# Optimization experiments

Measured on AMD Instinct MI355X. Metric: run time of the kernel, lower is better.

Reference implementation:

```python
import jax, jax.numpy as jnp
import numpy as np

NUM_LAYERS = 4
D_MODEL = 1024
N_HEAD = 16
D_FF = 1024
BATCH = 2
LONG = 2048
SHORT = 256


def setup_inputs() -> dict:
    key = jax.random.key(0)
    ks = jax.random.split(key, 6)
    s = 0.02
    L, D, F = NUM_LAYERS, D_MODEL, D_FF
    S = LONG + SHORT
    return {
        "x": jax.random.normal(ks[0], (BATCH, S, D), jnp.float32),
        "Wqkv": jax.random.normal(ks[1], (L, 3 * D, D), jnp.float32) * s,
        "bqkv": jnp.zeros((L, 3 * D), jnp.float32),
        "Wo": jax.random.normal(ks[2], (L, D, D), jnp.float32) * s,
        "bo": jnp.zeros((L, D), jnp.float32),
        "W1": jax.random.normal(ks[3], (L, F, D), jnp.float32) * s,
        "b1": jnp.zeros((L, F), jnp.float32),
        "W2": jax.random.normal(ks[4], (L, D, F), jnp.float32) * s,
        "b2": jnp.zeros((L, D), jnp.float32),
        "ln1_w": jnp.ones((L, D), jnp.float32),
        "ln1_b": jnp.zeros((L, D), jnp.float32),
        "ln2_w": jnp.ones((L, D), jnp.float32),
        "ln2_b": jnp.zeros((L, D), jnp.float32),
        "norm_w": jnp.ones((D,), jnp.float32),
        "norm_b": jnp.zeros((D,), jnp.float32),
        "long_seq_length": LONG,
        "num_short_seqs": SHORT,
    }


def _ln(x, w, b, eps=1e-5):
    m = jnp.mean(x, axis=-1, keepdims=True)
    v = jnp.mean(jnp.square(x - m), axis=-1, keepdims=True)
    return (x - m) * jax.lax.rsqrt(v + eps) * w + b


def _build_mask(long_seq_length, num_short_seqs, dtype):
    S = long_seq_length + num_short_seqs
    # long rows: attend only to long cols; short rows: long cols + own diag
    allowed = jnp.zeros((S, S), bool).at[:, :long_seq_length].set(True)
    sidx = jnp.arange(long_seq_length, S)
    allowed = allowed.at[sidx, sidx].set(True)
    return jnp.where(allowed, jnp.zeros((), dtype), -jnp.inf).astype(dtype)


def reference(x, Wqkv, bqkv, Wo, bo, W1, b1, W2, b2,
              ln1_w, ln1_b, ln2_w, ln2_b, norm_w, norm_b,
              long_seq_length, num_short_seqs):
    # dropout layers are treated as identity (eval / deterministic)
    B, S, D = x.shape
    H = N_HEAD
    dh = D // H
    scale = 1.0 / np.sqrt(dh)
    mask = _build_mask(long_seq_length, num_short_seqs, x.dtype)  # [S,S]

    for l in range(Wqkv.shape[0]):
        # --- nn.TransformerEncoderLayer (post-norm) ---
        qkv = jnp.einsum('bsd,ed->bse', x, Wqkv[l]) + bqkv[l]  # [B,S,3D]
        q, k, v = jnp.split(qkv, 3, axis=-1)
        q = q.reshape(B, S, H, dh).transpose(0, 2, 1, 3)
        k = k.reshape(B, S, H, dh).transpose(0, 2, 1, 3)
        v = v.reshape(B, S, H, dh).transpose(0, 2, 1, 3)
        scores = jnp.einsum('bhsd,bhtd->bhst', q, k) * scale + mask
        attn = jax.nn.softmax(scores, axis=-1)
        ctx = jnp.einsum('bhst,bhtd->bhsd', attn, v)
        ctx = ctx.transpose(0, 2, 1, 3).reshape(B, S, D)
        attn_out = jnp.einsum('bsd,ed->bse', ctx, Wo[l]) + bo[l]
        h = _ln(x + attn_out, ln1_w[l], ln1_b[l])
        ff = jnp.einsum('bsf,df->bsd',
                        jax.nn.relu(jnp.einsum('bsd,fd->bsf', h, W1[l]) + b1[l]),
                        W2[l]) + b2[l]
        y = _ln(h + ff, ln2_w[l], ln2_b[l])
        # --- outer residual + shared LayerNorm ---
        x = _ln(x + y, norm_w, norm_b)
    return x
```

## Files before the change

kernel.cpp:

```cpp
#include <hip/hip_runtime.h>

#define DEV __device__ __forceinline__

typedef short bf16x8 __attribute__((ext_vector_type(8)));
typedef short bf16x4_t __attribute__((ext_vector_type(4)));
typedef float f32x4 __attribute__((ext_vector_type(4)));

#define S_TOT 2304
#define D3    3072
#define NLONG 2048

DEV unsigned short f2b(float f) {
    union { float f; unsigned u; } v; v.f = f;
    unsigned r = v.u + 0x7fffu + ((v.u >> 16) & 1u);
    return (unsigned short)(r >> 16);
}
DEV float b2f(unsigned short u) {
    union { unsigned u; float f; } v; v.u = ((unsigned)u) << 16;
    return v.f;
}

#define GLL16(g, l) __builtin_amdgcn_global_load_lds( \
    (const __attribute__((address_space(1))) void*)(g), \
    (__attribute__((address_space(3))) void*)(l), 16, 0, 0)

DEV bf16x4_t tr_read(unsigned byteaddr) {
    bf16x4_t r;
    asm volatile("ds_read_b64_tr_b16 %0, %1" : "=v"(r) : "v"(byteaddr));
    return r;
}

__global__ __launch_bounds__(256) void k_cast(const float* __restrict__ in,
                                              unsigned short* __restrict__ out, long n) {
    long i = ((long)blockIdx.x * 256 + threadIdx.x) * 4;
    long stride = (long)gridDim.x * 1024;
    for (; i < n; i += stride) {
        float4 v = *(const float4*)(in + i);
        *(ushort4*)(out + i) = make_ushort4(f2b(v.x), f2b(v.y), f2b(v.z), f2b(v.w));
    }
}

__global__ __launch_bounds__(256) void k_castcopy(const float* __restrict__ in,
                                                  float* __restrict__ outf,
                                                  unsigned short* __restrict__ outb, long n) {
    long i = ((long)blockIdx.x * 256 + threadIdx.x) * 4;
    long stride = (long)gridDim.x * 1024;
    for (; i < n; i += stride) {
        float4 v = *(const float4*)(in + i);
        *(float4*)(outf + i) = v;
        *(ushort4*)(outb + i) = make_ushort4(f2b(v.x), f2b(v.y), f2b(v.z), f2b(v.w));
    }
}

template<int BN, int OBF, int RELU>
__global__ __launch_bounds__(256, 2) void k_gemm(const unsigned short* __restrict__ A,
                                                 const unsigned short* __restrict__ B,
                                                 const float* __restrict__ bias,
                                                 float* __restrict__ Cf,
                                                 unsigned short* __restrict__ Cb,
                                                 int M, int N, int K) {
    __shared__ unsigned short As[2][128 * 32];
    __shared__ unsigned short Bs[2][BN * 32];
    const int tid  = threadIdx.x;
    const int lane = tid & 63;
    const int wave = tid >> 6;
    const int g = lane >> 4, li = lane & 15;
    const int bm = blockIdx.x, bn = blockIdx.y;
    constexpr int WN = BN / 2;
    constexpr int NF = WN / 16;
    const int wm = (wave >> 1) * 64, wn = (wave & 1) * WN;

    f32x4 acc[4][NF] = {};

    const long abase = (long)bm * 128 * K;
    const long bbase = (long)bn * BN * K;
    const int srow = tid >> 2;
    const int scol = (tid & 3) * 8;

    auto stage = [&](int kt, int buf) {
        GLL16(A + abase + (long)srow * K + kt + scol, As[buf] + tid * 8);
        GLL16(A + abase + (long)(srow + 64) * K + kt + scol, As[buf] + (tid + 256) * 8);
        GLL16(B + bbase + (long)srow * K + kt + scol, Bs[buf] + tid * 8);
        if (BN == 128)
            GLL16(B + bbase + (long)(srow + 64) * K + kt + scol, Bs[buf] + (tid + 256) * 8);
    };

    const int nt = K / 32;
    stage(0, 0);
    for (int t = 0; t < nt; ++t) {
        __syncthreads();
        if (t + 1 < nt) stage((t + 1) * 32, (t + 1) & 1);
        const unsigned short* Ab = As[t & 1];
        const unsigned short* Bb = Bs[t & 1];
        bf16x8 af[4], bfr[NF];
#pragma unroll
        for (int mf = 0; mf < 4; ++mf)
            af[mf] = *(const bf16x8*)(Ab + (wm + mf * 16 + li) * 32 + g * 8);
#pragma unroll
        for (int nf = 0; nf < NF; ++nf)
            bfr[nf] = *(const bf16x8*)(Bb + (wn + nf * 16 + li) * 32 + g * 8);
#pragma unroll
        for (int mf = 0; mf < 4; ++mf)
#pragma unroll
            for (int nf = 0; nf < NF; ++nf)
                acc[mf][nf] = __builtin_amdgcn_mfma_f32_16x16x32_bf16(af[mf], bfr[nf], acc[mf][nf], 0, 0, 0);
    }

#pragma unroll
    for (int nf = 0; nf < NF; ++nf) {
        int col = bn * BN + wn + nf * 16 + li;
        float bv = bias[col];
#pragma unroll
        for (int mf = 0; mf < 4; ++mf) {
#pragma unroll
            for (int i = 0; i < 4; ++i) {
                int row = bm * 128 + wm + mf * 16 + g * 4 + i;
                float v = acc[mf][nf][i] + bv;
                if (RELU) v = fmaxf(v, 0.f);
                if (OBF) Cb[(long)row * N + col] = f2b(v);
                else     Cf[(long)row * N + col] = v;
            }
        }
    }
}

__global__ __launch_bounds__(256, 2) void k_attn(const unsigned short* __restrict__ qkv,
                                                 unsigned short* __restrict__ ctx) {
    __shared__ unsigned short Ks[2][64 * 64];
    __shared__ unsigned short Vt[2][64 * 72];
    __shared__ unsigned short Ps[4][2048];

    const int tid  = threadIdx.x;
    const int lane = tid & 63, wave = tid >> 6;
    const int g = lane >> 4, li = lane & 15;
    const int bq = blockIdx.x, h = blockIdx.y, b = blockIdx.z;
    const int q0 = bq * 128 + wave * 32;

    const long baseQ = ((long)b * S_TOT) * D3 + h * 64;
    const long baseK = baseQ + 1024;
    const long baseV = baseQ + 2048;

    bf16x8 qf[2][2];
#pragma unroll
    for (int mf = 0; mf < 2; ++mf)
#pragma unroll
        for (int kk = 0; kk < 2; ++kk)
            qf[mf][kk] = *(const bf16x8*)(qkv + baseQ + (long)(q0 + mf * 16 + li) * D3 + kk * 32 + g * 8);

    f32x4 O[2][4] = {};
    float psum[2][4] = {};

    unsigned short* Pw = Ps[wave];
    const unsigned pwb = (unsigned)(size_t)Pw + lane * 8u;

    auto stageK = [&](int kt, int buf) {
#pragma unroll
        for (int r = 0; r < 2; ++r) {
            int s = tid + r * 256;
            int kr = s >> 3, si = s & 7;
            GLL16(qkv + baseK + (long)(kt + kr) * D3 + ((si ^ (kr & 7)) * 8), Ks[buf] + s * 8);
        }
    };
    auto loadV = [&](int kt, ushort4* vr) {
        int t0 = (tid & 15) * 4, d0 = (tid >> 4) * 4;
        const unsigned short* vp = qkv + baseV + (long)(kt + t0) * D3 + d0;
        vr[0] = *(const ushort4*)(vp);
        vr[1] = *(const ushort4*)(vp + D3);
        vr[2] = *(const ushort4*)(vp + 2 * D3);
        vr[3] = *(const ushort4*)(vp + 3 * D3);
    };
    auto writeVt = [&](const ushort4* vr, int buf) {
        int t0 = (tid & 15) * 4, d0 = (tid >> 4) * 4;
        unsigned short* Vb = Vt[buf];
        *(ushort4*)(Vb + (d0 + 0) * 72 + t0) = make_ushort4(vr[0].x, vr[1].x, vr[2].x, vr[3].x);
        *(ushort4*)(Vb + (d0 + 1) * 72 + t0) = make_ushort4(vr[0].y, vr[1].y, vr[2].y, vr[3].y);
        *(ushort4*)(Vb + (d0 + 2) * 72 + t0) = make_ushort4(vr[0].z, vr[1].z, vr[2].z, vr[3].z);
        *(ushort4*)(Vb + (d0 + 3) * 72 + t0) = make_ushort4(vr[0].w, vr[1].w, vr[2].w, vr[3].w);
    };

    auto compute = [&](int cur) {
        f32x4 sc[2][4] = {};
        const unsigned short* Kb = Ks[cur];
#pragma unroll
        for (int kk = 0; kk < 2; ++kk) {
            bf16x8 kf[4];
#pragma unroll
            for (int nf = 0; nf < 4; ++nf) {
                int kr = nf * 16 + li;
                int slot = (kk * 4 + g) ^ (kr & 7);
                kf[nf] = *(const bf16x8*)(Kb + kr * 64 + slot * 8);
            }
#pragma unroll
            for (int mf = 0; mf < 2; ++mf)
#pragma unroll
                for (int nf = 0; nf < 4; ++nf)
                    sc[mf][nf] = __builtin_amdgcn_mfma_f32_16x16x32_bf16(qf[mf][kk], kf[nf], sc[mf][nf], 0, 0, 0);
        }
#pragma unroll
        for (int mf = 0; mf < 2; ++mf) {
#pragma unroll
            for (int nf = 0; nf < 4; ++nf) {
                float p0 = __expf(sc[mf][nf][0] * 0.125f);
                float p1 = __expf(sc[mf][nf][1] * 0.125f);
                float p2 = __expf(sc[mf][nf][2] * 0.125f);
                float p3 = __expf(sc[mf][nf][3] * 0.125f);
                psum[mf][0] += p0; psum[mf][1] += p1;
                psum[mf][2] += p2; psum[mf][3] += p3;
                unsigned lo, hi;
                asm("v_cvt_pk_bf16_f32 %0, %1, %2" : "=v"(lo) : "v"(p0), "v"(p1));
                asm("v_cvt_pk_bf16_f32 %0, %1, %2" : "=v"(hi) : "v"(p2), "v"(p3));
                unsigned idx = (unsigned)(g * 4 + (li & 3) * 16 + (nf * 2 + (li >> 3)) * 64 +
                                          ((li >> 2) & 1) * 512 + mf * 1024);
                *(uint2*)(Pw + idx) = make_uint2(lo, hi);
            }
        }
        asm volatile("" ::: "memory");
        bf16x4_t pa[2][2][2];
#pragma unroll
        for (int mf = 0; mf < 2; ++mf)
#pragma unroll
            for (int kk = 0; kk < 2; ++kk) {
                unsigned base = pwb + 2u * (unsigned)(kk * 256 + mf * 1024);
                pa[mf][kk][0] = tr_read(base);
                pa[mf][kk][1] = tr_read(base + 1024u);
            }
        asm volatile("s_waitcnt lgkmcnt(0)" ::: "memory");
        __builtin_amdgcn_sched_barrier(0);
        const unsigned short* Vb = Vt[cur];
#pragma unroll
        for (int kk = 0; kk < 2; ++kk) {
            bf16x8 vf[4];
#pragma unroll
            for (int nfd = 0; nfd < 4; ++nfd)
                vf[nfd] = *(const bf16x8*)(Vb + (nfd * 16 + li) * 72 + kk * 32 + g * 8);
#pragma unroll
            for (int mf = 0; mf < 2; ++mf) {
                bf16x8 paf = __builtin_shufflevector(pa[mf][kk][0], pa[mf][kk][1],
                                                     0, 1, 2, 3, 4, 5, 6, 7);
#pragma unroll
                for (int nfd = 0; nfd < 4; ++nfd)
                    O[mf][nfd] = __builtin_amdgcn_mfma_f32_16x16x32_bf16(paf, vf[nfd], O[mf][nfd], 0, 0, 0);
            }
        }
    };

    ushort4 vrA[4], vrB[4];
    stageK(0, 0);
    loadV(0, vrA);
    for (int ti = 0; ti < 32; ti += 2) {
        writeVt(vrA, 0);
        __syncthreads();
        if (ti + 1 < 32) { stageK((ti + 1) * 64, 1); loadV((ti + 1) * 64, vrB); }
        compute(0);
        writeVt(vrB, 1);
        __syncthreads();
        if (ti + 2 < 32) { stageK((ti + 2) * 64, 0); loadV((ti + 2) * 64, vrA); }
        compute(1);
    }

    float lrow[2][4];
#pragma unroll
    for (int mf = 0; mf < 2; ++mf)
#pragma unroll
        for (int i = 0; i < 4; ++i) {
            float s = psum[mf][i];
#pragma unroll
            for (int off = 1; off < 16; off <<= 1) s += __shfl_xor(s, off);
            lrow[mf][i] = s;
        }

    if (q0 >= NLONG) {
#pragma unroll
        for (int mf = 0; mf < 2; ++mf) {
#pragma unroll
            for (int i = 0; i < 4; ++i) {
                int q = q0 + mf * 16 + g * 4 + i;
                ushort4 q4 = *(const ushort4*)(qkv + baseQ + (long)q * D3 + li * 4);
                ushort4 k4 = *(const ushort4*)(qkv + baseK + (long)q * D3 + li * 4);
                float p = b2f(q4.x) * b2f(k4.x) + b2f(q4.y) * b2f(k4.y) +
                          b2f(q4.z) * b2f(k4.z) + b2f(q4.w) * b2f(k4.w);
#pragma unroll
                for (int off = 1; off < 16; off <<= 1) p += __shfl_xor(p, off);
                float pe = __expf(p * 0.125f);
                lrow[mf][i] += pe;
#pragma unroll
                for (int nfd = 0; nfd < 4; ++nfd) {
                    float vd = b2f(qkv[baseV + (long)q * D3 + nfd * 16 + li]);
                    O[mf][nfd][i] += pe * vd;
                }
            }
        }
    }

#pragma unroll
    for (int mf = 0; mf < 2; ++mf) {
#pragma unroll
        for (int i = 0; i < 4; ++i) {
            float inv = 1.0f / lrow[mf][i];
            int q = q0 + mf * 16 + g * 4 + i;
            long obase = ((long)b * S_TOT + q) * 1024 + h * 64;
#pragma unroll
            for (int nfd = 0; nfd < 4; ++nfd)
                ctx[obase + nfd * 16 + li] = f2b(O[mf][nfd][i] * inv);
        }
    }
}

DEV void block_reduce2(float& sum, float& sq, float* sbuf, int tid) {
#pragma unroll
    for (int off = 32; off > 0; off >>= 1) {
        sum += __shfl_xor(sum, off);
        sq  += __shfl_xor(sq, off);
    }
    __syncthreads();
    if ((tid & 63) == 0) { sbuf[(tid >> 6) * 2] = sum; sbuf[(tid >> 6) * 2 + 1] = sq; }
    __syncthreads();
    sum = sbuf[0] + sbuf[2] + sbuf[4] + sbuf[6];
    sq  = sbuf[1] + sbuf[3] + sbuf[5] + sbuf[7];
}

__global__ __launch_bounds__(256) void k_ln_resid(const float* __restrict__ xa,
                                                  const float* __restrict__ xb,
                                                  const float* __restrict__ w,
                                                  const float* __restrict__ bs,
                                                  float* __restrict__ outf,
                                                  unsigned short* __restrict__ outb) {
    __shared__ float sbuf[8];
    const int tid = threadIdx.x;
    const long base = (long)blockIdx.x * 1024 + tid * 4;
    float4 a = *(const float4*)(xa + base);
    float4 b4 = *(const float4*)(xb + base);
    float4 s = make_float4(a.x + b4.x, a.y + b4.y, a.z + b4.z, a.w + b4.w);
    float sum = s.x + s.y + s.z + s.w;
    float sq = s.x * s.x + s.y * s.y + s.z * s.z + s.w * s.w;
    block_reduce2(sum, sq, sbuf, tid);
    float mean = sum * (1.f / 1024.f);
    float rstd = rsqrtf(sq * (1.f / 1024.f) - mean * mean + 1e-5f);
    float4 wv = *(const float4*)(w + tid * 4);
    float4 bv = *(const float4*)(bs + tid * 4);
    float4 o = make_float4((s.x - mean) * rstd * wv.x + bv.x,
                           (s.y - mean) * rstd * wv.y + bv.y,
                           (s.z - mean) * rstd * wv.z + bv.z,
                           (s.w - mean) * rstd * wv.w + bv.w);
    *(float4*)(outf + base) = o;
    *(ushort4*)(outb + base) = make_ushort4(f2b(o.x), f2b(o.y), f2b(o.z), f2b(o.w));
}

__global__ __launch_bounds__(256) void k_ln_double(const float* __restrict__ h,
                                                   const float* __restrict__ ff,
                                                   const float* __restrict__ x,
                                                   const float* __restrict__ w2,
                                                   const float* __restrict__ bb2,
                                                   const float* __restrict__ nw,
                                                   const float* __restrict__ nb,
                                                   float* __restrict__ outf,
                                                   unsigned short* __restrict__ outb) {
    __shared__ float sbuf[8];
    const int tid = threadIdx.x;
    const long base = (long)blockIdx.x * 1024 + tid * 4;
    float4 hv = *(const float4*)(h + base);
    float4 fv = *(const float4*)(ff + base);
    float4 s = make_float4(hv.x + fv.x, hv.y + fv.y, hv.z + fv.z, hv.w + fv.w);
    float sum = s.x + s.y + s.z + s.w;
    float sq = s.x * s.x + s.y * s.y + s.z * s.z + s.w * s.w;
    block_reduce2(sum, sq, sbuf, tid);
    float mean = sum * (1.f / 1024.f);
    float rstd = rsqrtf(sq * (1.f / 1024.f) - mean * mean + 1e-5f);
    float4 wv = *(const float4*)(w2 + tid * 4);
    float4 bv = *(const float4*)(bb2 + tid * 4);
    float4 y = make_float4((s.x - mean) * rstd * wv.x + bv.x,
                           (s.y - mean) * rstd * wv.y + bv.y,
                           (s.z - mean) * rstd * wv.z + bv.z,
                           (s.w - mean) * rstd * wv.w + bv.w);
    float4 xv = *(const float4*)(x + base);
    float4 t = make_float4(xv.x + y.x, xv.y + y.y, xv.z + y.z, xv.w + y.w);
    sum = t.x + t.y + t.z + t.w;
    sq = t.x * t.x + t.y * t.y + t.z * t.z + t.w * t.w;
    block_reduce2(sum, sq, sbuf, tid);
    mean = sum * (1.f / 1024.f);
    rstd = rsqrtf(sq * (1.f / 1024.f) - mean * mean + 1e-5f);
    float4 nwv = *(const float4*)(nw + tid * 4);
    float4 nbv = *(const float4*)(nb + tid * 4);
    float4 o = make_float4((t.x - mean) * rstd * nwv.x + nbv.x,
                           (t.y - mean) * rstd * nwv.y + nbv.y,
                           (t.z - mean) * rstd * nwv.z + nbv.z,
                           (t.w - mean) * rstd * nwv.w + nbv.w);
    *(float4*)(outf + base) = o;
    *(ushort4*)(outb + base) = make_ushort4(f2b(o.x), f2b(o.y), f2b(o.z), f2b(o.w));
}

extern "C" void kernel_launch(void* const* d_in, const int* in_sizes, int n_in,
                              void* d_out, int out_size, void* d_ws, size_t ws_size,
                              hipStream_t stream) {
    (void)in_sizes; (void)n_in; (void)out_size; (void)ws_size;
    const float* x_in  = (const float*)d_in[0];
    const float* Wqkv  = (const float*)d_in[1];
    const float* bqkv  = (const float*)d_in[2];
    const float* Wo    = (const float*)d_in[3];
    const float* bo    = (const float*)d_in[4];
    const float* W1    = (const float*)d_in[5];
    const float* b1    = (const float*)d_in[6];
    const float* W2    = (const float*)d_in[7];
    const float* b2    = (const float*)d_in[8];
    const float* ln1w  = (const float*)d_in[9];
    const float* ln1b  = (const float*)d_in[10];
    const float* ln2w  = (const float*)d_in[11];
    const float* ln2b  = (const float*)d_in[12];
    const float* nw    = (const float*)d_in[13];
    const float* nb    = (const float*)d_in[14];
    float* xf = (float*)d_out;

    char* p = (char*)d_ws;
    auto alloc = [&](size_t bytes) { char* r = p; p += (bytes + 255) & ~(size_t)255; return r; };
    unsigned short* wqkv_b = (unsigned short*)alloc(12582912UL * 2);
    unsigned short* wo_b   = (unsigned short*)alloc(4194304UL * 2);
    unsigned short* w1_b   = (unsigned short*)alloc(4194304UL * 2);
    unsigned short* w2_b   = (unsigned short*)alloc(4194304UL * 2);
    unsigned short* x_b    = (unsigned short*)alloc(4718592UL * 2);
    unsigned short* qkv_b  = (unsigned short*)alloc(14155776UL * 2);
    unsigned short* ctx_b  = (unsigned short*)alloc(4718592UL * 2);
    unsigned short* h_b    = (unsigned short*)alloc(4718592UL * 2);
    unsigned short* ff1_b  = (unsigned short*)alloc(4718592UL * 2);
    float* h_f   = (float*)alloc(4718592UL * 4);
    float* tmp_f = (float*)alloc(4718592UL * 4);

    k_cast<<<4096, 256, 0, stream>>>(Wqkv, wqkv_b, 12582912L);
    k_cast<<<2048, 256, 0, stream>>>(Wo, wo_b, 4194304L);
    k_cast<<<2048, 256, 0, stream>>>(W1, w1_b, 4194304L);
    k_cast<<<2048, 256, 0, stream>>>(W2, w2_b, 4194304L);
    k_castcopy<<<2048, 256, 0, stream>>>(x_in, xf, x_b, 4718592L);

    for (int l = 0; l < 4; ++l) {
        k_gemm<128, 1, 0><<<dim3(36, 24), 256, 0, stream>>>(x_b, wqkv_b + (size_t)l * 3145728,
                                                            bqkv + l * 3072, nullptr, qkv_b, 4608, 3072, 1024);
        k_attn<<<dim3(18, 16, 2), 256, 0, stream>>>(qkv_b, ctx_b);
        k_gemm<64, 0, 0><<<dim3(36, 16), 256, 0, stream>>>(ctx_b, wo_b + (size_t)l * 1048576,
                                                           bo + l * 1024, tmp_f, nullptr, 4608, 1024, 1024);
        k_ln_resid<<<4608, 256, 0, stream>>>(xf, tmp_f, ln1w + l * 1024, ln1b + l * 1024, h_f, h_b);
        k_gemm<64, 1, 1><<<dim3(36, 16), 256, 0, stream>>>(h_b, w1_b + (size_t)l * 1048576,
                                                           b1 + l * 1024, nullptr, ff1_b, 4608, 1024, 1024);
        k_gemm<64, 0, 0><<<dim3(36, 16), 256, 0, stream>>>(ff1_b, w2_b + (size_t)l * 1048576,
                                                           b2 + l * 1024, tmp_f, nullptr, 4608, 1024, 1024);
        k_ln_double<<<4608, 256, 0, stream>>>(h_f, tmp_f, xf, ln2w + l * 1024, ln2b + l * 1024,
                                              nw, nb, xf, x_b);
    }
}
```

Before: 1.149 ms.

## Split-K attention with combine kernel, triple-buffer GEMM, and swizzle workgroup order

The attention kernel now splits the 2048 long keys into two chunks across more blocks. It writes unnormalised partial outputs and row sums, and a new combine kernel merges them and adds the short-sequence diagonal term. V is now loaded straight into LDS with global_load_lds and read with transposed LDS reads, which replaces the register transpose. The GEMM moves to a 3-stage LDS pipeline with explicit vmcnt waits, higher occupancy hints and an XCD-aware block ID remap. Together these aim to raise parallelism and overlap memory with MFMA work, at the cost of extra fp32 partial traffic, which reuses the h_f/tmp_f buffers.

```diff
diff --git a/kernel.cpp b/kernel.cpp
--- a/kernel.cpp
+++ b/kernel.cpp
@@ -9,6 +9,7 @@
 #define S_TOT 2304
 #define D3    3072
 #define NLONG 2048
+#define OSTRIDE 4718592L
 
 DEV unsigned short f2b(float f) {
     union { float f; unsigned u; } v; v.f = f;
@@ -53,19 +54,26 @@
 }
 
 template<int BN, int OBF, int RELU>
-__global__ __launch_bounds__(256, 2) void k_gemm(const unsigned short* __restrict__ A,
-                                                 const unsigned short* __restrict__ B,
-                                                 const float* __restrict__ bias,
-                                                 float* __restrict__ Cf,
-                                                 unsigned short* __restrict__ Cb,
-                                                 int M, int N, int K) {
-    __shared__ unsigned short As[2][128 * 32];
-    __shared__ unsigned short Bs[2][BN * 32];
+__global__ __launch_bounds__(256, BN == 128 ? 3 : 4)
+void k_gemm(const unsigned short* __restrict__ A,
+            const unsigned short* __restrict__ B,
+            const float* __restrict__ bias,
+            float* __restrict__ Cf,
+            unsigned short* __restrict__ Cb,
+            int M, int N, int K) {
+    __shared__ unsigned short As[3][128 * 32];
+    __shared__ unsigned short Bs[3][BN * 32];
     const int tid  = threadIdx.x;
     const int lane = tid & 63;
     const int wave = tid >> 6;
     const int g = lane >> 4, li = lane & 15;
-    const int bm = blockIdx.x, bn = blockIdx.y;
+
+    const int nbm = gridDim.x;
+    const int nwg = nbm * gridDim.y;
+    int id = blockIdx.x + blockIdx.y * nbm;
+    if ((nwg & 7) == 0) id = (id & 7) * (nwg >> 3) + (id >> 3);
+    const int bm = id % nbm, bn = id / nbm;
+
     constexpr int WN = BN / 2;
     constexpr int NF = WN / 16;
     const int wm = (wave >> 1) * 64, wn = (wave & 1) * WN;
@@ -87,11 +95,17 @@
 
     const int nt = K / 32;
     stage(0, 0);
+    stage(32, 1);
+    if constexpr (BN == 128) asm volatile("s_waitcnt vmcnt(4)" ::: "memory");
+    else                     asm volatile("s_waitcnt vmcnt(3)" ::: "memory");
+
     for (int t = 0; t < nt; ++t) {
-        __syncthreads();
-        if (t + 1 < nt) stage((t + 1) * 32, (t + 1) & 1);
-        const unsigned short* Ab = As[t & 1];
-        const unsigned short* Bb = Bs[t & 1];
+        __builtin_amdgcn_s_barrier();
+        __builtin_amdgcn_sched_barrier(0);
+        asm volatile("" ::: "memory");
+        if (t + 2 < nt) stage((t + 2) * 32, (t + 2) % 3);
+        const unsigned short* Ab = As[t % 3];
+        const unsigned short* Bb = Bs[t % 3];
         bf16x8 af[4], bfr[NF];
 #pragma unroll
         for (int mf = 0; mf < 4; ++mf)
@@ -104,6 +118,12 @@
 #pragma unroll
             for (int nf = 0; nf < NF; ++nf)
                 acc[mf][nf] = __builtin_amdgcn_mfma_f32_16x16x32_bf16(af[mf], bfr[nf], acc[mf][nf], 0, 0, 0);
+        if (t + 2 < nt) {
+            if constexpr (BN == 128) asm volatile("s_waitcnt vmcnt(4)" ::: "memory");
+            else                     asm volatile("s_waitcnt vmcnt(3)" ::: "memory");
+        } else {
+            asm volatile("s_waitcnt vmcnt(0)" ::: "memory");
+        }
     }
 
 #pragma unroll
@@ -124,17 +144,20 @@
     }
 }
 
-__global__ __launch_bounds__(256, 2) void k_attn(const unsigned short* __restrict__ qkv,
-                                                 unsigned short* __restrict__ ctx) {
-    __shared__ unsigned short Ks[2][64 * 64];
-    __shared__ unsigned short Vt[2][64 * 72];
+__global__ __launch_bounds__(256, 3) void k_attn(const unsigned short* __restrict__ qkv,
+                                                 float* __restrict__ Opart,
+                                                 float* __restrict__ lpart) {
+    __shared__ unsigned short Ks[2][4096];
+    __shared__ unsigned short Vt[2][4096];
     __shared__ unsigned short Ps[4][2048];
 
     const int tid  = threadIdx.x;
     const int lane = tid & 63, wave = tid >> 6;
     const int g = lane >> 4, li = lane & 15;
-    const int bq = blockIdx.x, h = blockIdx.y, b = blockIdx.z;
+    const int bq = blockIdx.x, h = blockIdx.y;
+    const int b = blockIdx.z & 1, chunk = blockIdx.z >> 1;
     const int q0 = bq * 128 + wave * 32;
+    const int koff = chunk * 1024;
 
     const long baseQ = ((long)b * S_TOT) * D3 + h * 64;
     const long baseK = baseQ + 1024;
@@ -153,29 +176,21 @@
     unsigned short* Pw = Ps[wave];
     const unsigned pwb = (unsigned)(size_t)Pw + lane * 8u;
 
-    auto stageK = [&](int kt, int buf) {
+    auto stage = [&](int ti, int buf) {
+        const int kt = koff + ti * 64;
 #pragma unroll
         for (int r = 0; r < 2; ++r) {
             int s = tid + r * 256;
             int kr = s >> 3, si = s & 7;
             GLL16(qkv + baseK + (long)(kt + kr) * D3 + ((si ^ (kr & 7)) * 8), Ks[buf] + s * 8);
         }
-    };
-    auto loadV = [&](int kt, ushort4* vr) {
-        int t0 = (tid & 15) * 4, d0 = (tid >> 4) * 4;
-        const unsigned short* vp = qkv + baseV + (long)(kt + t0) * D3 + d0;
-        vr[0] = *(const ushort4*)(vp);
-        vr[1] = *(const ushort4*)(vp + D3);
-        vr[2] = *(const ushort4*)(vp + 2 * D3);
-        vr[3] = *(const ushort4*)(vp + 3 * D3);
-    };
-    auto writeVt = [&](const ushort4* vr, int buf) {
-        int t0 = (tid & 15) * 4, d0 = (tid >> 4) * 4;
-        unsigned short* Vb = Vt[buf];
-        *(ushort4*)(Vb + (d0 + 0) * 72 + t0) = make_ushort4(vr[0].x, vr[1].x, vr[2].x, vr[3].x);
-        *(ushort4*)(Vb + (d0 + 1) * 72 + t0) = make_ushort4(vr[0].y, vr[1].y, vr[2].y, vr[3].y);
-        *(ushort4*)(Vb + (d0 + 2) * 72 + t0) = make_ushort4(vr[0].z, vr[1].z, vr[2].z, vr[3].z);
-        *(ushort4*)(Vb + (d0 + 3) * 72 + t0) = make_ushort4(vr[0].w, vr[1].w, vr[2].w, vr[3].w);
+#pragma unroll
+        for (int r = 0; r < 2; ++r) {
+            int i = tid + r * 256;
+            int vt = ((i >> 5) << 2) + ((i & 7) >> 1);
+            int vd = (((i >> 3) & 3) << 4) + ((i & 1) << 3);
+            GLL16(qkv + baseV + (long)(kt + vt) * D3 + vd, Vt[buf] + i * 8);
+        }
     };
 
     auto compute = [&](int cur) {
@@ -224,38 +239,39 @@
                 pa[mf][kk][0] = tr_read(base);
                 pa[mf][kk][1] = tr_read(base + 1024u);
             }
+        const unsigned vtb = (unsigned)(size_t)(&Vt[cur][0]) + lane * 8u + (unsigned)(lane >> 4) * 896u;
+        bf16x4_t vr[2][4][2];
+#pragma unroll
+        for (int kk = 0; kk < 2; ++kk)
+#pragma unroll
+            for (int nfd = 0; nfd < 4; ++nfd) {
+                unsigned base = vtb + (unsigned)(kk * 4096 + nfd * 128);
+                vr[kk][nfd][0] = tr_read(base);
+                vr[kk][nfd][1] = tr_read(base + 512u);
+            }
         asm volatile("s_waitcnt lgkmcnt(0)" ::: "memory");
         __builtin_amdgcn_sched_barrier(0);
-        const unsigned short* Vb = Vt[cur];
 #pragma unroll
         for (int kk = 0; kk < 2; ++kk) {
-            bf16x8 vf[4];
-#pragma unroll
-            for (int nfd = 0; nfd < 4; ++nfd)
-                vf[nfd] = *(const bf16x8*)(Vb + (nfd * 16 + li) * 72 + kk * 32 + g * 8);
 #pragma unroll
             for (int mf = 0; mf < 2; ++mf) {
                 bf16x8 paf = __builtin_shufflevector(pa[mf][kk][0], pa[mf][kk][1],
                                                      0, 1, 2, 3, 4, 5, 6, 7);
 #pragma unroll
-                for (int nfd = 0; nfd < 4; ++nfd)
-                    O[mf][nfd] = __builtin_amdgcn_mfma_f32_16x16x32_bf16(paf, vf[nfd], O[mf][nfd], 0, 0, 0);
+                for (int nfd = 0; nfd < 4; ++nfd) {
+                    bf16x8 vf = __builtin_shufflevector(vr[kk][nfd][0], vr[kk][nfd][1],
+                                                        0, 1, 2, 3, 4, 5, 6, 7);
+                    O[mf][nfd] = __builtin_amdgcn_mfma_f32_16x16x32_bf16(paf, vf, O[mf][nfd], 0, 0, 0);
+                }
             }
         }
     };
 
-    ushort4 vrA[4], vrB[4];
-    stageK(0, 0);
-    loadV(0, vrA);
-    for (int ti = 0; ti < 32; ti += 2) {
-        writeVt(vrA, 0);
+    stage(0, 0);
+    for (int ti = 0; ti < 16; ++ti) {
         __syncthreads();
-        if (ti + 1 < 32) { stageK((ti + 1) * 64, 1); loadV((ti + 1) * 64, vrB); }
-        compute(0);
-        writeVt(vrB, 1);
-        __syncthreads();
-        if (ti + 2 < 32) { stageK((ti + 2) * 64, 0); loadV((ti + 2) * 64, vrA); }
-        compute(1);
+        if (ti + 1 < 16) stage(ti + 1, (ti + 1) & 1);
+        compute(ti & 1);
     }
 
     float lrow[2][4];
@@ -269,41 +285,58 @@
             lrow[mf][i] = s;
         }
 
-    if (q0 >= NLONG) {
-#pragma unroll
-        for (int mf = 0; mf < 2; ++mf) {
-#pragma unroll
-            for (int i = 0; i < 4; ++i) {
-                int q = q0 + mf * 16 + g * 4 + i;
-                ushort4 q4 = *(const ushort4*)(qkv + baseQ + (long)q * D3 + li * 4);
-                ushort4 k4 = *(const ushort4*)(qkv + baseK + (long)q * D3 + li * 4);
-                float p = b2f(q4.x) * b2f(k4.x) + b2f(q4.y) * b2f(k4.y) +
-                          b2f(q4.z) * b2f(k4.z) + b2f(q4.w) * b2f(k4.w);
-#pragma unroll
-                for (int off = 1; off < 16; off <<= 1) p += __shfl_xor(p, off);
-                float pe = __expf(p * 0.125f);
-                lrow[mf][i] += pe;
-#pragma unroll
-                for (int nfd = 0; nfd < 4; ++nfd) {
-                    float vd = b2f(qkv[baseV + (long)q * D3 + nfd * 16 + li]);
-                    O[mf][nfd][i] += pe * vd;
-                }
-            }
-        }
-    }
-
+    float* Od = Opart + (long)chunk * OSTRIDE;
+    const long bh = ((long)b * 16 + h) * 2304;
 #pragma unroll
     for (int mf = 0; mf < 2; ++mf) {
 #pragma unroll
         for (int i = 0; i < 4; ++i) {
-            float inv = 1.0f / lrow[mf][i];
             int q = q0 + mf * 16 + g * 4 + i;
-            long obase = ((long)b * S_TOT + q) * 1024 + h * 64;
+            long ob = (bh + q) * 64;
 #pragma unroll
             for (int nfd = 0; nfd < 4; ++nfd)
-                ctx[obase + nfd * 16 + li] = f2b(O[mf][nfd][i] * inv);
-        }
-    }
+                Od[ob + nfd * 16 + li] = O[mf][nfd][i];
+            if (li == 0)
+                lpart[((long)(chunk * 2 + b) * 16 + h) * 2304 + q] = lrow[mf][i];
+        }
+    }
+}
+
+__global__ __launch_bounds__(256) void k_comb(const unsigned short* __restrict__ qkv,
+                                              const float* __restrict__ Opart,
+                                              const float* __restrict__ lpart,
+                                              unsigned short* __restrict__ ctx) {
+    const int q = blockIdx.x % S_TOT;
+    const int b = blockIdx.x / S_TOT;
+    const int tid = threadIdx.x;
+    const int h = tid >> 4;
+    const int d0 = (tid & 15) * 4;
+
+    const long idx = (((long)b * 16 + h) * 2304 + q) * 64 + d0;
+    float4 O1 = *(const float4*)(Opart + idx);
+    float4 O2 = *(const float4*)(Opart + OSTRIDE + idx);
+    float den = lpart[((long)b * 16 + h) * 2304 + q] +
+                lpart[((long)(2 + b) * 16 + h) * 2304 + q];
+    float4 num = make_float4(O1.x + O2.x, O1.y + O2.y, O1.z + O2.z, O1.w + O2.w);
+
+    if (q >= NLONG) {
+        const long qb = ((long)b * S_TOT + q) * D3 + h * 64 + d0;
+        ushort4 qv = *(const ushort4*)(qkv + qb);
+        ushort4 kv = *(const ushort4*)(qkv + qb + 1024);
+        float dot = b2f(qv.x) * b2f(kv.x) + b2f(qv.y) * b2f(kv.y) +
+                    b2f(qv.z) * b2f(kv.z) + b2f(qv.w) * b2f(kv.w);
+#pragma unroll
+        for (int off = 1; off < 16; off <<= 1) dot += __shfl_xor(dot, off);
+        float pe = __expf(dot * 0.125f);
+        ushort4 vv = *(const ushort4*)(qkv + qb + 2048);
+        num.x += pe * b2f(vv.x); num.y += pe * b2f(vv.y);
+        num.z += pe * b2f(vv.z); num.w += pe * b2f(vv.w);
+        den += pe;
+    }
+    float inv = 1.0f / den;
+    long ob = ((long)b * S_TOT + q) * 1024 + h * 64 + d0;
+    *(ushort4*)(ctx + ob) = make_ushort4(f2b(num.x * inv), f2b(num.y * inv),
+                                         f2b(num.z * inv), f2b(num.w * inv));
 }
 
 DEV void block_reduce2(float& sum, float& sq, float* sbuf, int tid) {
@@ -421,8 +454,10 @@
     unsigned short* ctx_b  = (unsigned short*)alloc(4718592UL * 2);
     unsigned short* h_b    = (unsigned short*)alloc(4718592UL * 2);
     unsigned short* ff1_b  = (unsigned short*)alloc(4718592UL * 2);
-    float* h_f   = (float*)alloc(4718592UL * 4);
-    float* tmp_f = (float*)alloc(4718592UL * 4);
+    float* of_f  = (float*)alloc(2 * 4718592UL * 4);
+    float* h_f   = of_f;
+    float* tmp_f = of_f + OSTRIDE;
+    float* lpart = (float*)alloc(147456UL * 4);
 
     k_cast<<<4096, 256, 0, stream>>>(Wqkv, wqkv_b, 12582912L);
     k_cast<<<2048, 256, 0, stream>>>(Wo, wo_b, 4194304L);
@@ -433,7 +468,8 @@
     for (int l = 0; l < 4; ++l) {
         k_gemm<128, 1, 0><<<dim3(36, 24), 256, 0, stream>>>(x_b, wqkv_b + (size_t)l * 3145728,
                                                             bqkv + l * 3072, nullptr, qkv_b, 4608, 3072, 1024);
-        k_attn<<<dim3(18, 16, 2), 256, 0, stream>>>(qkv_b, ctx_b);
+        k_attn<<<dim3(18, 16, 4), 256, 0, stream>>>(qkv_b, of_f, lpart);
+        k_comb<<<4608, 256, 0, stream>>>(qkv_b, of_f, lpart, ctx_b);
         k_gemm<64, 0, 0><<<dim3(36, 16), 256, 0, stream>>>(ctx_b, wo_b + (size_t)l * 1048576,
                                                            bo + l * 1024, tmp_f, nullptr, 4608, 1024, 1024);
         k_ln_resid<<<4608, 256, 0, stream>>>(xf, tmp_f, ln1w + l * 1024, ln1b + l * 1024, h_f, h_b);
```

Measured after the change: 1.121 ms. 2.4% less time.
